# Performance work log

Hardware: AMD Instinct MI355X
Metric: run time of the kernel (lower is better)

The kernel has to match this reference:

```python
import jax, jax.numpy as jnp
import numpy as np

B, BOND, N, ATOM, UNITS = 256, 5, 128, 64, 128


def setup_inputs() -> dict:
    key = jax.random.key(0)
    k1, k2, k3 = jax.random.split(key, 3)
    adjacency = jax.random.uniform(k1, (B, BOND, N, N), dtype=jnp.float32)
    features = jax.random.normal(k2, (B, N, ATOM), dtype=jnp.float32)
    # per-sample unique kernel: (global_batch, bond_dim, atom_dim, units)
    kernel = jax.random.normal(k3, (B, BOND, ATOM, UNITS), dtype=jnp.float32) * 0.05
    return {"adjacency": adjacency, "features": features, "kernel": kernel}


def reference(adjacency, features, kernel):
    # aggregate neighbors per bond type: [B, bond, N, atom]
    x = jnp.einsum('bemn,bnd->bemd', adjacency, features)
    # per-sample, per-bond linear transform: [B, bond, N, units]
    x = jnp.einsum('bemd,bedu->bemu', x, kernel)
    # reduce over bond types, then activation: [B, N, units]
    return jax.nn.relu(jnp.sum(x, axis=1))
```

## Files before the change

kernel.cpp:

```cpp
#include <hip/hip_runtime.h>


typedef __attribute__((ext_vector_type(8))) short s8v;
typedef __attribute__((ext_vector_type(4))) float f4v;

__device__ __forceinline__ short f2bf(float f) {
    unsigned u = __builtin_bit_cast(unsigned, f);
    u += 0x7FFFu + ((u >> 16) & 1u);
    return (short)(u >> 16);
}

__global__ __launch_bounds__(256, 4)
void rgc_kernel(const float* __restrict__ adj,
                const float* __restrict__ feat,
                const float* __restrict__ ker,
                float* __restrict__ out)
{
    __shared__ __align__(16) short featT[64][136];
    __shared__ __align__(16) short YB[4][16][72];

    const int b    = blockIdx.x >> 2;
    const int rg   = blockIdx.x & 3;
    const int tid  = threadIdx.x;
    const int w    = tid >> 6;
    const int mw   = w >> 1;
    const int uw   = w & 1;
    const int lane = tid & 63;
    const int c16  = lane & 15;
    const int quad = lane >> 4;

    const float* adjB  = adj  + (size_t)b * (5 * 128 * 128);
    const float* featB = feat + (size_t)b * (128 * 64);
    const float* kerB  = ker  + (size_t)b * (5 * 64 * 128);
    float*       outB  = out  + (size_t)b * (128 * 128);

    {
        f4v fv[8];
        #pragma unroll
        for (int i = 0; i < 8; ++i)
            fv[i] = *(const f4v*)(featB + (i * 256 + tid) * 4);
        #pragma unroll
        for (int i = 0; i < 8; ++i) {
            int g = i * 256 + tid;
            int n = g >> 4, d0 = (g & 15) << 2;
            #pragma unroll
            for (int j = 0; j < 4; ++j)
                featT[d0 + j][n] = f2bf(fv[i][j]);
        }
    }
    __syncthreads();

    const int rowS = 32 * rg + 16 * mw;
    const float* ap0 = adjB + (rowS + c16) * 128 + 8 * quad;
    const float* kp0 = kerB + (8 * quad) * 128 + 64 * uw + c16;
    short (*YBw)[72] = YB[w];

    f4v oacc[4] = {};

    for (int e = 0; e < 5; ++e) {
        const float* ap = ap0 + e * (128 * 128);
        f4v a0[4], a1[4];
        #pragma unroll
        for (int k16 = 0; k16 < 4; ++k16) {
            a0[k16] = *(const f4v*)(ap + 32 * k16);
            a1[k16] = *(const f4v*)(ap + 32 * k16 + 4);
        }

        f4v yacc[4] = {};
        #pragma unroll
        for (int k16 = 0; k16 < 4; ++k16) {
            s8v af;
            #pragma unroll
            for (int j = 0; j < 4; ++j) af[j] = f2bf(a0[k16][j]);
            #pragma unroll
            for (int j = 0; j < 4; ++j) af[4 + j] = f2bf(a1[k16][j]);
            #pragma unroll
            for (int d16 = 0; d16 < 4; ++d16) {
                s8v bf = *(const s8v*)&featT[16 * d16 + c16][32 * k16 + 8 * quad];
                yacc[d16] = __builtin_amdgcn_mfma_f32_16x16x32_bf16(af, bf, yacc[d16], 0, 0, 0);
            }
        }

        #pragma unroll
        for (int d16 = 0; d16 < 4; ++d16)
            #pragma unroll
            for (int r = 0; r < 4; ++r)
                YBw[4 * quad + r][16 * d16 + c16] = f2bf(yacc[d16][r]);
        s8v y0 = *(const s8v*)&YBw[c16][8 * quad];
        s8v y1 = *(const s8v*)&YBw[c16][32 + 8 * quad];

        const float* kp = kp0 + e * (64 * 128);
        #pragma unroll
        for (int u16 = 0; u16 < 4; ++u16) {
            s8v b0, b1;
            #pragma unroll
            for (int j = 0; j < 8; ++j) {
                b0[j] = f2bf(kp[j * 128 + 16 * u16]);
                b1[j] = f2bf(kp[(32 + j) * 128 + 16 * u16]);
            }
            oacc[u16] = __builtin_amdgcn_mfma_f32_16x16x32_bf16(y0, b0, oacc[u16], 0, 0, 0);
            oacc[u16] = __builtin_amdgcn_mfma_f32_16x16x32_bf16(y1, b1, oacc[u16], 0, 0, 0);
        }
    }

    #pragma unroll
    for (int u16 = 0; u16 < 4; ++u16)
        #pragma unroll
        for (int r = 0; r < 4; ++r)
            outB[(rowS + 4 * quad + r) * 128 + 64 * uw + 16 * u16 + c16] =
                fmaxf(oacc[u16][r], 0.f);
}

extern "C" void kernel_launch(void* const* d_in, const int* in_sizes, int n_in,
                              void* d_out, int out_size, void* d_ws, size_t ws_size,
                              hipStream_t stream)
{
    const float* adj  = (const float*)d_in[0];
    const float* feat = (const float*)d_in[1];
    const float* ker  = (const float*)d_in[2];
    rgc_kernel<<<1024, 256, 0, stream>>>(adj, feat, ker, (float*)d_out);
}
```

Measured before the change: 192.9 us.

## Stage kernel weights in double-buffered shared memory with 512-thread blocks

Blocks grow to 512 threads, and each block now covers 64 rows of one sample, so the grid shrinks to 512 blocks. The per-bond kernel slice is converted to bf16 once into XOR-swizzled shared memory. Each block prefetches the next bond's slice into registers and a second buffer while computing the current one. This removes redundant strided global loads of the kernel by every wave. Feature and Y staging use swizzled layouts to cut bank conflicts. The cost is per-bond block barriers, more shared memory per block (which may reduce occupancy), and half as many blocks.

```diff
diff --git a/kernel.cpp b/kernel.cpp
--- a/kernel.cpp
+++ b/kernel.cpp
@@ -10,17 +10,18 @@
     return (short)(u >> 16);
 }
 
-__global__ __launch_bounds__(256, 4)
+__global__ __launch_bounds__(512, 4)
 void rgc_kernel(const float* __restrict__ adj,
                 const float* __restrict__ feat,
                 const float* __restrict__ ker,
                 float* __restrict__ out)
 {
-    __shared__ __align__(16) short featT[64][136];
-    __shared__ __align__(16) short YB[4][16][72];
+    __shared__ __align__(16) short featT_s[64 * 128];
+    __shared__ __align__(16) short kerT_s[2][128 * 64];
+    __shared__ __align__(16) short YB_s[8][16 * 64];
 
-    const int b    = blockIdx.x >> 2;
-    const int rg   = blockIdx.x & 3;
+    const int bs   = blockIdx.x & 255;
+    const int half = blockIdx.x >> 8;
     const int tid  = threadIdx.x;
     const int w    = tid >> 6;
     const int mw   = w >> 1;
@@ -29,41 +30,64 @@
     const int c16  = lane & 15;
     const int quad = lane >> 4;
 
-    const float* adjB  = adj  + (size_t)b * (5 * 128 * 128);
-    const float* featB = feat + (size_t)b * (128 * 64);
-    const float* kerB  = ker  + (size_t)b * (5 * 64 * 128);
-    float*       outB  = out  + (size_t)b * (128 * 128);
+    const float* adjB  = adj  + (size_t)bs * (5 * 128 * 128);
+    const float* featB = feat + (size_t)bs * (128 * 64);
+    const float* kerB  = ker  + (size_t)bs * (5 * 64 * 128);
+    float*       outB  = out  + (size_t)bs * (128 * 128);
 
+    const int rowS = 64 * half + 16 * mw;
+
+    #pragma unroll
+    for (int s = 0; s < 2; ++s) {
+        const int d  = lane;
+        const int cn = 8 * s + w;
+        float v[8];
+        #pragma unroll
+        for (int j = 0; j < 8; ++j) v[j] = featB[(8 * cn + j) * 64 + d];
+        s8v fr;
+        #pragma unroll
+        for (int j = 0; j < 8; ++j) fr[j] = f2bf(v[j]);
+        *(s8v*)&featT_s[d * 128 + ((cn ^ (d & 7)) << 3)] = fr;
+    }
     {
-        f4v fv[8];
+        const int u = tid & 127;
         #pragma unroll
-        for (int i = 0; i < 8; ++i)
-            fv[i] = *(const f4v*)(featB + (i * 256 + tid) * 4);
-        #pragma unroll
-        for (int i = 0; i < 8; ++i) {
-            int g = i * 256 + tid;
-            int n = g >> 4, d0 = (g & 15) << 2;
+        for (int s = 0; s < 2; ++s) {
+            const int cd = 4 * s + mw;
+            float v[8];
             #pragma unroll
-            for (int j = 0; j < 4; ++j)
-                featT[d0 + j][n] = f2bf(fv[i][j]);
+            for (int j = 0; j < 8; ++j) v[j] = kerB[(8 * cd + j) * 128 + u];
+            s8v fr;
+            #pragma unroll
+            for (int j = 0; j < 8; ++j) fr[j] = f2bf(v[j]);
+            *(s8v*)&kerT_s[0][u * 64 + (((cd ^ (u & 7))) << 3)] = fr;
         }
     }
     __syncthreads();
 
-    const int rowS = 32 * rg + 16 * mw;
-    const float* ap0 = adjB + (rowS + c16) * 128 + 8 * quad;
-    const float* kp0 = kerB + (8 * quad) * 128 + 64 * uw + c16;
-    short (*YBw)[72] = YB[w];
-
     f4v oacc[4] = {};
 
+    #pragma unroll
     for (int e = 0; e < 5; ++e) {
-        const float* ap = ap0 + e * (128 * 128);
+        const int buf = e & 1;
+
+        const float* ap = adjB + e * 16384 + (rowS + c16) * 128 + 8 * quad;
         f4v a0[4], a1[4];
         #pragma unroll
         for (int k16 = 0; k16 < 4; ++k16) {
             a0[k16] = *(const f4v*)(ap + 32 * k16);
             a1[k16] = *(const f4v*)(ap + 32 * k16 + 4);
+        }
+        float kv[2][8];
+        const int u = tid & 127;
+        if (e < 4) {
+            #pragma unroll
+            for (int s = 0; s < 2; ++s) {
+                const int cd = 4 * s + mw;
+                #pragma unroll
+                for (int j = 0; j < 8; ++j)
+                    kv[s][j] = kerB[(e + 1) * 8192 + (8 * cd + j) * 128 + u];
+            }
         }
 
         f4v yacc[4] = {};
@@ -76,31 +100,47 @@
             for (int j = 0; j < 4; ++j) af[4 + j] = f2bf(a1[k16][j]);
             #pragma unroll
             for (int d16 = 0; d16 < 4; ++d16) {
-                s8v bf = *(const s8v*)&featT[16 * d16 + c16][32 * k16 + 8 * quad];
+                const int d = 16 * d16 + c16;
+                s8v bf = *(const s8v*)
+                    &featT_s[d * 128 + (((4 * k16 + quad) ^ (d & 7)) << 3)];
                 yacc[d16] = __builtin_amdgcn_mfma_f32_16x16x32_bf16(af, bf, yacc[d16], 0, 0, 0);
             }
         }
 
+        if (e < 4) {
+            #pragma unroll
+            for (int s = 0; s < 2; ++s) {
+                const int cd = 4 * s + mw;
+                s8v fr;
+                #pragma unroll
+                for (int j = 0; j < 8; ++j) fr[j] = f2bf(kv[s][j]);
+                *(s8v*)&kerT_s[buf ^ 1][u * 64 + ((cd ^ (u & 7)) << 3)] = fr;
+            }
+        }
+
+        short* YBw = YB_s[w];
         #pragma unroll
-        for (int d16 = 0; d16 < 4; ++d16)
+        for (int d16 = 0; d16 < 4; ++d16) {
+            const int ch = 2 * d16 + (c16 >> 3);
             #pragma unroll
-            for (int r = 0; r < 4; ++r)
-                YBw[4 * quad + r][16 * d16 + c16] = f2bf(yacc[d16][r]);
-        s8v y0 = *(const s8v*)&YBw[c16][8 * quad];
-        s8v y1 = *(const s8v*)&YBw[c16][32 + 8 * quad];
+            for (int r = 0; r < 4; ++r) {
+                const int m = 4 * quad + r;
+                YBw[m * 64 + ((ch ^ (m & 7)) << 3) + (c16 & 7)] = f2bf(yacc[d16][r]);
+            }
+        }
+        s8v y0 = *(const s8v*)&YBw[c16 * 64 + ((quad ^ (c16 & 7)) << 3)];
+        s8v y1 = *(const s8v*)&YBw[c16 * 64 + (((4 + quad) ^ (c16 & 7)) << 3)];
 
-        const float* kp = kp0 + e * (64 * 128);
         #pragma unroll
         for (int u16 = 0; u16 < 4; ++u16) {
-            s8v b0, b1;
-            #pragma unroll
-            for (int j = 0; j < 8; ++j) {
-                b0[j] = f2bf(kp[j * 128 + 16 * u16]);
-                b1[j] = f2bf(kp[(32 + j) * 128 + 16 * u16]);
-            }
+            const int uc = 64 * uw + 16 * u16 + c16;
+            s8v b0 = *(const s8v*)&kerT_s[buf][uc * 64 + ((quad ^ (uc & 7)) << 3)];
+            s8v b1 = *(const s8v*)&kerT_s[buf][uc * 64 + (((4 + quad) ^ (uc & 7)) << 3)];
             oacc[u16] = __builtin_amdgcn_mfma_f32_16x16x32_bf16(y0, b0, oacc[u16], 0, 0, 0);
             oacc[u16] = __builtin_amdgcn_mfma_f32_16x16x32_bf16(y1, b1, oacc[u16], 0, 0, 0);
         }
+
+        if (e < 4) __syncthreads();
     }
 
     #pragma unroll
@@ -118,5 +158,5 @@
     const float* adj  = (const float*)d_in[0];
     const float* feat = (const float*)d_in[1];
     const float* ker  = (const float*)d_in[2];
-    rgc_kernel<<<1024, 256, 0, stream>>>(adj, feat, ker, (float*)d_out);
+    rgc_kernel<<<512, 512, 0, stream>>>(adj, feat, ker, (float*)d_out);
 }
```

Measured after the change: 173.0 us. -10.3%, faster.

## Stage kernel weights through swizzled LDS with register prefetch, remap block order

Applied to the files above, without the earlier changes.

Each bond's kernel slice is now loaded with coalesced vector loads, converted to bf16 and stored transposed into an XOR-swizzled shared-memory tile, where it was previously read with strided scalar global loads per lane. The next bond's kernel is prefetched into registers during the current bond's compute. featT and the Y staging buffer switch from padded arrays to swizzled layouts, bf16 packing is done two values at a time, and blocks are remapped so batch varies fastest. The cost is two extra __syncthreads per bond, more LDS per block, and higher register pressure, which may reduce occupancy.

```diff
diff --git a/kernel.cpp b/kernel.cpp
--- a/kernel.cpp
+++ b/kernel.cpp
@@ -4,10 +4,25 @@
 typedef __attribute__((ext_vector_type(8))) short s8v;
 typedef __attribute__((ext_vector_type(4))) float f4v;
 
-__device__ __forceinline__ short f2bf(float f) {
+__device__ __forceinline__ unsigned bfr(float f) {
     unsigned u = __builtin_bit_cast(unsigned, f);
     u += 0x7FFFu + ((u >> 16) & 1u);
-    return (short)(u >> 16);
+    return u >> 16;
+}
+__device__ __forceinline__ unsigned pk2(float a, float b) {
+    return bfr(a) | (bfr(b) << 16);
+}
+__device__ __forceinline__ s8v mk_frag(f4v lo, f4v hi) {
+    union { unsigned u[4]; s8v s; } r;
+    r.u[0] = pk2(lo[0], lo[1]); r.u[1] = pk2(lo[2], lo[3]);
+    r.u[2] = pk2(hi[0], hi[1]); r.u[3] = pk2(hi[2], hi[3]);
+    return r.s;
+}
+__device__ __forceinline__ int adrF(int d, int n) {
+    return d * 128 + (((n >> 3) ^ (d & 7)) << 3) + (n & 7);
+}
+__device__ __forceinline__ int adrK(int u, int d) {
+    return u * 64 + (((d >> 3) ^ (u & 7)) << 3) + (d & 7);
 }
 
 __global__ __launch_bounds__(256, 4)
@@ -16,67 +31,83 @@
                 const float* __restrict__ ker,
                 float* __restrict__ out)
 {
-    __shared__ __align__(16) short featT[64][136];
-    __shared__ __align__(16) short YB[4][16][72];
+    __shared__ __align__(16) short featT[64 * 128];
+    __shared__ __align__(16) short kerT[128 * 64];
+    __shared__ __align__(16) short YB[4][16 * 64];
 
-    const int b    = blockIdx.x >> 2;
-    const int rg   = blockIdx.x & 3;
+    const int bs   = blockIdx.x & 255;
+    const int Q    = blockIdx.x >> 8;
     const int tid  = threadIdx.x;
     const int w    = tid >> 6;
-    const int mw   = w >> 1;
-    const int uw   = w & 1;
+    const int mt   = w >> 1;
+    const int uh   = w & 1;
     const int lane = tid & 63;
     const int c16  = lane & 15;
     const int quad = lane >> 4;
 
-    const float* adjB  = adj  + (size_t)b * (5 * 128 * 128);
-    const float* featB = feat + (size_t)b * (128 * 64);
-    const float* kerB  = ker  + (size_t)b * (5 * 64 * 128);
-    float*       outB  = out  + (size_t)b * (128 * 128);
+    const float* adjB  = adj  + (size_t)bs * (5 * 128 * 128);
+    const float* featB = feat + (size_t)bs * (128 * 64);
+    const float* kerB  = ker  + (size_t)bs * (5 * 64 * 128);
+    float*       outB  = out  + (size_t)bs * (128 * 128);
 
     {
-        f4v fv[8];
+        const int sn = tid & 127, sdh = tid >> 7;
+        const float* fp = featB + sn * 64 + sdh * 32;
+        f4v v[8];
+        #pragma unroll
+        for (int i = 0; i < 8; ++i) v[i] = *(const f4v*)(fp + 4 * i);
         #pragma unroll
         for (int i = 0; i < 8; ++i)
-            fv[i] = *(const f4v*)(featB + (i * 256 + tid) * 4);
+            #pragma unroll
+            for (int j = 0; j < 4; ++j) {
+                const int d = 32 * sdh + 4 * i + j;
+                featT[adrF(d, sn)] = (short)bfr(v[i][j]);
+            }
+    }
+    {
+        const float* kp = kerB + lane * 128 + 32 * w;
+        f4v v[8];
         #pragma unroll
-        for (int i = 0; i < 8; ++i) {
-            int g = i * 256 + tid;
-            int n = g >> 4, d0 = (g & 15) << 2;
+        for (int i = 0; i < 8; ++i) v[i] = *(const f4v*)(kp + 4 * i);
+        #pragma unroll
+        for (int i = 0; i < 8; ++i)
             #pragma unroll
-            for (int j = 0; j < 4; ++j)
-                featT[d0 + j][n] = f2bf(fv[i][j]);
-        }
+            for (int j = 0; j < 4; ++j) {
+                const int u = 32 * w + 4 * i + j;
+                kerT[adrK(u, lane)] = (short)bfr(v[i][j]);
+            }
     }
     __syncthreads();
 
-    const int rowS = 32 * rg + 16 * mw;
+    const int rowS = 32 * Q + 16 * mt;
     const float* ap0 = adjB + (rowS + c16) * 128 + 8 * quad;
-    const float* kp0 = kerB + (8 * quad) * 128 + 64 * uw + c16;
-    short (*YBw)[72] = YB[w];
+    short* YBw = YB[w];
 
     f4v oacc[4] = {};
 
     for (int e = 0; e < 5; ++e) {
-        const float* ap = ap0 + e * (128 * 128);
+        const float* ap = ap0 + e * 16384;
         f4v a0[4], a1[4];
         #pragma unroll
         for (int k16 = 0; k16 < 4; ++k16) {
             a0[k16] = *(const f4v*)(ap + 32 * k16);
             a1[k16] = *(const f4v*)(ap + 32 * k16 + 4);
         }
+        f4v kv[8];
+        if (e < 4) {
+            const float* kp = kerB + (e + 1) * 8192 + lane * 128 + 32 * w;
+            #pragma unroll
+            for (int i = 0; i < 8; ++i) kv[i] = *(const f4v*)(kp + 4 * i);
+        }
 
         f4v yacc[4] = {};
         #pragma unroll
         for (int k16 = 0; k16 < 4; ++k16) {
-            s8v af;
-            #pragma unroll
-            for (int j = 0; j < 4; ++j) af[j] = f2bf(a0[k16][j]);
-            #pragma unroll
-            for (int j = 0; j < 4; ++j) af[4 + j] = f2bf(a1[k16][j]);
+            s8v af = mk_frag(a0[k16], a1[k16]);
             #pragma unroll
             for (int d16 = 0; d16 < 4; ++d16) {
-                s8v bf = *(const s8v*)&featT[16 * d16 + c16][32 * k16 + 8 * quad];
+                const int d = 16 * d16 + c16;
+                s8v bf = *(const s8v*)&featT[d * 128 + (((4 * k16 + quad) ^ (d & 7)) << 3)];
                 yacc[d16] = __builtin_amdgcn_mfma_f32_16x16x32_bf16(af, bf, yacc[d16], 0, 0, 0);
             }
         }
@@ -84,22 +115,32 @@
         #pragma unroll
         for (int d16 = 0; d16 < 4; ++d16)
             #pragma unroll
-            for (int r = 0; r < 4; ++r)
-                YBw[4 * quad + r][16 * d16 + c16] = f2bf(yacc[d16][r]);
-        s8v y0 = *(const s8v*)&YBw[c16][8 * quad];
-        s8v y1 = *(const s8v*)&YBw[c16][32 + 8 * quad];
+            for (int r = 0; r < 4; ++r) {
+                const int m = 4 * quad + r;
+                YBw[adrK(m, 16 * d16 + c16)] = (short)bfr(yacc[d16][r]);
+            }
+        s8v y0 = *(const s8v*)&YBw[c16 * 64 + ((quad ^ (c16 & 7)) << 3)];
+        s8v y1 = *(const s8v*)&YBw[c16 * 64 + (((4 + quad) ^ (c16 & 7)) << 3)];
 
-        const float* kp = kp0 + e * (64 * 128);
         #pragma unroll
         for (int u16 = 0; u16 < 4; ++u16) {
-            s8v b0, b1;
-            #pragma unroll
-            for (int j = 0; j < 8; ++j) {
-                b0[j] = f2bf(kp[j * 128 + 16 * u16]);
-                b1[j] = f2bf(kp[(32 + j) * 128 + 16 * u16]);
-            }
+            const int uc = 64 * uh + 16 * u16 + c16;
+            s8v b0 = *(const s8v*)&kerT[uc * 64 + ((quad ^ (uc & 7)) << 3)];
+            s8v b1 = *(const s8v*)&kerT[uc * 64 + (((4 + quad) ^ (uc & 7)) << 3)];
             oacc[u16] = __builtin_amdgcn_mfma_f32_16x16x32_bf16(y0, b0, oacc[u16], 0, 0, 0);
             oacc[u16] = __builtin_amdgcn_mfma_f32_16x16x32_bf16(y1, b1, oacc[u16], 0, 0, 0);
+        }
+
+        if (e < 4) {
+            __syncthreads();
+            #pragma unroll
+            for (int i = 0; i < 8; ++i)
+                #pragma unroll
+                for (int j = 0; j < 4; ++j) {
+                    const int u = 32 * w + 4 * i + j;
+                    kerT[adrK(u, lane)] = (short)bfr(kv[i][j]);
+                }
+            __syncthreads();
         }
     }
 
@@ -107,7 +148,7 @@
     for (int u16 = 0; u16 < 4; ++u16)
         #pragma unroll
         for (int r = 0; r < 4; ++r)
-            outB[(rowS + 4 * quad + r) * 128 + 64 * uw + 16 * u16 + c16] =
+            outB[(rowS + 4 * quad + r) * 128 + 64 * uh + 16 * u16 + c16] =
                 fmaxf(oacc[u16][r], 0.f);
 }
 
```

Result: faster. 188.1 us (-2.5%).
